# Optimization experiments

Hardware: AMD Instinct MI355X
Metric: run time of the kernel (lower is better)

Reference implementation:

```python
import jax, jax.numpy as jnp
import numpy as np

N = 20000
E = 320000
IN_C, HID, OUT_C = 128, 64, 32
H12, H3 = 4, 1  # heads for conv1/conv2 and conv3
NEG_SLOPE = 0.2


def _glorot(key, shape):
    fan_in, fan_out = shape[0], shape[-1]
    lim = (6.0 / (fan_in + fan_out)) ** 0.5
    return jax.random.uniform(key, shape, jnp.float32, -lim, lim)


def setup_inputs() -> dict:
    key = jax.random.key(0)
    ks = jax.random.split(key, 16)
    x = jax.random.normal(ks[0], (N, IN_C), jnp.float32)
    edge_index = jax.random.randint(ks[1], (2, E), 0, N, jnp.int64)
    p = {
        'W1': _glorot(ks[2], (IN_C, H12 * HID)),
        'as1': _glorot(ks[3], (H12, HID)), 'ad1': _glorot(ks[4], (H12, HID)),
        'b1': jnp.zeros((HID,), jnp.float32),
        'W2': _glorot(ks[5], (HID, H12 * HID)),
        'as2': _glorot(ks[6], (H12, HID)), 'ad2': _glorot(ks[7], (H12, HID)),
        'b2': jnp.zeros((HID,), jnp.float32),
        'W3': _glorot(ks[8], (HID, H3 * OUT_C)),
        'as3': _glorot(ks[9], (H3, OUT_C)), 'ad3': _glorot(ks[10], (H3, OUT_C)),
        'b3': jnp.zeros((OUT_C,), jnp.float32),
        'Wm': _glorot(ks[11], (OUT_C, OUT_C)), 'bm': jnp.zeros((OUT_C,), jnp.float32),
        'Wv': _glorot(ks[12], (OUT_C, OUT_C)), 'bv': jnp.zeros((OUT_C,), jnp.float32),
    }
    return dict(x=x, edge_index=edge_index, **p)


def gat_layer(x, src, dst, W, a_src, a_dst, b, heads, out_c):
    # x: [N, in_c] -> h: [N, H, C]
    h = (x @ W).reshape(-1, heads, out_c)
    alpha_s = jnp.einsum('nhc,hc->nh', h, a_src)  # [N,H]
    alpha_d = jnp.einsum('nhc,hc->nh', h, a_dst)
    e = jax.nn.leaky_relu(alpha_s[src] + alpha_d[dst], NEG_SLOPE)  # [E',H]
    # segment softmax over incoming edges of each dst node
    m = jax.ops.segment_max(e, dst, num_segments=N)
    p = jnp.exp(e - m[dst])
    s = jax.ops.segment_sum(p, dst, num_segments=N)
    alpha = p / (s[dst] + 1e-16)  # [E',H]
    msg = h[src] * alpha[:, :, None]  # [E',H,C]
    out = jax.ops.segment_sum(msg, dst, num_segments=N)  # [N,H,C]
    return out.mean(axis=1) + b  # concat=False -> mean over heads


def reference(x, edge_index, W1, as1, ad1, b1, W2, as2, ad2, b2,
              W3, as3, ad3, b3, Wm, bm, Wv, bv):
    # PyG GATConv default: add self loops
    loop = jnp.arange(N, dtype=edge_index.dtype)
    src = jnp.concatenate([edge_index[0], loop])
    dst = jnp.concatenate([edge_index[1], loop])

    h = jax.nn.relu(gat_layer(x, src, dst, W1, as1, ad1, b1, H12, HID))
    h = jax.nn.relu(gat_layer(h, src, dst, W2, as2, ad2, b2, H12, HID))
    z = gat_layer(h, src, dst, W3, as3, ad3, b3, H3, OUT_C)

    z_mean = z @ Wm + bm
    z_var = jnp.clip(jnp.exp(z @ Wv + bv), 1e-8, 100.0)
    return (z_mean, z_var, z)
```

## Files before the change

### kernel.cpp

```cpp
#include <hip/hip_runtime.h>
#include <hip/hip_bf16.h>

typedef unsigned short ushortT;
typedef short short8 __attribute__((ext_vector_type(8)));
typedef unsigned short ushort8v __attribute__((ext_vector_type(8)));
typedef float float4v __attribute__((ext_vector_type(4)));

constexpr int Nn   = 20000;
constexpr int Ee   = 320000;
constexpr int EP   = Ee + Nn;
constexpr float NSL = 0.2f;
constexpr int CAP  = 128;

__device__ __forceinline__ float b2f(__hip_bfloat16 v) { return __bfloat162float(v); }
__device__ __forceinline__ float bits2f(unsigned short u) {
    __hip_bfloat16 b; *(unsigned short*)&b = u; return __bfloat162float(b);
}
__device__ __forceinline__ unsigned short f2bits(float v) {
    __hip_bfloat16 b = __float2bfloat16(v); return *(unsigned short*)&b;
}
__device__ __forceinline__ float ldf(const void* p, size_t i, int bf) {
    return bf ? __bfloat162float(((const __hip_bfloat16*)p)[i])
              : ((const float*)p)[i];
}
__device__ __forceinline__ void stf(void* p, size_t i, float v, int bf) {
    if (bf) ((__hip_bfloat16*)p)[i] = __float2bfloat16(v);
    else    ((float*)p)[i] = v;
}

__global__ void probe_k(const int* __restrict__ ei, const unsigned* __restrict__ xbits,
                        int* __restrict__ eflag, int* __restrict__ fflag,
                        int* __restrict__ cnt) {
    int gi = blockIdx.x * 256 + threadIdx.x;
    if (gi < Nn) cnt[gi] = 0;
    if (blockIdx.x != 0) return;
    __shared__ int bad, c_s;
    if (threadIdx.x == 0) { bad = 0; c_s = 0; }
    __syncthreads();
    for (int i = threadIdx.x; i < 1024; i += 256)
        if (ei[2 * i + 1] != 0) bad = 1;
    int c = 0;
    for (int i = threadIdx.x; i < 512; i += 256) {
        unsigned e = (xbits[i] >> 7) & 0xFFu;
        if (e >= 110u && e <= 135u) ++c;
    }
    atomicAdd(&c_s, c);
    __syncthreads();
    if (threadIdx.x == 0) {
        *eflag = bad ? 0 : 1;
        *fflag = (c_s > 384) ? 1 : 0;
    }
}

__device__ __forceinline__ void load_edge(const int* __restrict__ ei, int sh, int e,
                                          int& si, int& di) {
    if (e < Ee) {
        si = ei[(size_t)e << sh];
        di = ei[(size_t)(Ee + e) << sh];
    } else {
        si = di = e - Ee;
    }
}

__global__ void prep_k(const void* __restrict__ W1, const void* __restrict__ W2,
                       ushortT* __restrict__ WT1, ushortT* __restrict__ WT2,
                       const int* __restrict__ fflag) {
    const int bf = *fflag;
    int idx = blockIdx.x * 256 + threadIdx.x;
    if (idx < 256 * 128) {
        int j = idx >> 7, k = idx & 127;
        WT1[idx] = f2bits(ldf(W1, (size_t)k * 256 + j, bf));
    } else {
        int i2 = idx - 256 * 128;
        if (i2 < 256 * 64) {
            int j = i2 >> 6, k = i2 & 63;
            WT2[i2] = f2bits(ldf(W2, (size_t)k * 256 + j, bf));
        }
    }
}

__global__ void scatter_k(const int* __restrict__ ei, const int* __restrict__ eflag,
                          int* __restrict__ cnt, int* __restrict__ csr) {
    int e = blockIdx.x * 256 + threadIdx.x;
    if (e >= EP) return;
    int sh = *eflag, si, di;
    load_edge(ei, sh, e, si, di);
    int pos = atomicAdd(cnt + di, 1);
    if (pos < CAP) csr[di * CAP + pos] = si;
}

template <int XMODE, int INC>
__global__ __launch_bounds__(256) void gemm_mfma(const void* __restrict__ xg,
                                                 const ushortT* __restrict__ WT,
                                                 ushortT* __restrict__ h,
                                                 const void* __restrict__ avs,
                                                 const void* __restrict__ avd,
                                                 float* __restrict__ as_, float* __restrict__ ad_,
                                                 const int* __restrict__ fflag) {
    constexpr int SW = INC + 8, SX = INC + 8, CPR = INC / 8;
    const int bf  = *fflag;
    const int xbf = (XMODE == 0) ? bf : 1;
    __shared__ ushortT wt_s[128 * SW];
    __shared__ ushortT xs[64 * SX];
    __shared__ float av_s[2][128];
    const int base = blockIdx.x * 64;
    const int jh   = blockIdx.y;
    const ushortT* WTg = WT + (size_t)jh * 128 * INC;
    for (int ch = threadIdx.x; ch < 128 * CPR; ch += 256) {
        int j = ch / CPR, kc = (ch - j * CPR) * 8;
        *(short8*)(wt_s + j * SW + kc) = *(const short8*)(WTg + j * INC + kc);
    }
    for (int ch = threadIdx.x; ch < 64 * CPR; ch += 256) {
        int nl = ch / CPR, kc = (ch - nl * CPR) * 8;
        int node = base + nl;
        short8 v = {0, 0, 0, 0, 0, 0, 0, 0};
        if (node < Nn) {
            if (xbf) {
                v = *(const short8*)((const ushortT*)xg + (size_t)node * INC + kc);
            } else {
                const float* xf = (const float*)xg + (size_t)node * INC + kc;
#pragma unroll
                for (int i = 0; i < 8; ++i) v[i] = (short)f2bits(xf[i]);
            }
        }
        *(short8*)(xs + nl * SX + kc) = v;
    }
    if (threadIdx.x < 128) {
        av_s[0][threadIdx.x] = ldf(avs, jh * 128 + threadIdx.x, bf);
        av_s[1][threadIdx.x] = ldf(avd, jh * 128 + threadIdx.x, bf);
    }
    __syncthreads();
    const int lane = threadIdx.x & 63, w = threadIdx.x >> 6;
    const int ln = lane & 15, quad = lane >> 4;
    float4v acc[8];
#pragma unroll
    for (int T = 0; T < 8; ++T) acc[T] = (float4v){0.f, 0.f, 0.f, 0.f};
#pragma unroll
    for (int ks = 0; ks < INC / 32; ++ks) {
        const int kb = ks * 32 + quad * 8;
        const short8 b = *(const short8*)(xs + (w * 16 + ln) * SX + kb);
#pragma unroll
        for (int T = 0; T < 8; ++T) {
            const short8 a = *(const short8*)(wt_s + (T * 16 + ln) * SW + kb);
            acc[T] = __builtin_amdgcn_mfma_f32_16x16x32_bf16(a, b, acc[T], 0, 0, 0);
        }
    }
    const int node = base + w * 16 + ln;
    const bool live = (node < Nn);
    ushortT* hn = h + (size_t)node * 256 + jh * 128;
    float pas0 = 0, pas1 = 0, pad0 = 0, pad1 = 0;
#pragma unroll
    for (int T = 0; T < 8; ++T) {
        const int jl = T * 16 + quad * 4;
        ushort4 pk;
        pk.x = f2bits(acc[T][0]); pk.y = f2bits(acc[T][1]);
        pk.z = f2bits(acc[T][2]); pk.w = f2bits(acc[T][3]);
        if (live) *(ushort4*)(hn + jl) = pk;
#pragma unroll
        for (int r = 0; r < 4; ++r) {
            const float v = acc[T][r];
            const float was = av_s[0][jl + r], wad = av_s[1][jl + r];
            if (T < 4) { pas0 = fmaf(v, was, pas0); pad0 = fmaf(v, wad, pad0); }
            else       { pas1 = fmaf(v, was, pas1); pad1 = fmaf(v, wad, pad1); }
        }
    }
#pragma unroll
    for (int off = 16; off < 64; off <<= 1) {
        pas0 += __shfl_xor(pas0, off, 64);
        pas1 += __shfl_xor(pas1, off, 64);
        pad0 += __shfl_xor(pad0, off, 64);
        pad1 += __shfl_xor(pad1, off, 64);
    }
    if (lane < 16 && live) {
        as_[node * 4 + jh * 2]     = pas0;
        as_[node * 4 + jh * 2 + 1] = pas1;
        ad_[node * 4 + jh * 2]     = pad0;
        ad_[node * 4 + jh * 2 + 1] = pad1;
    }
}

__global__ __launch_bounds__(256) void gemm_small(const float* __restrict__ x,
                                                  const void* __restrict__ W,
                                                  __hip_bfloat16* __restrict__ h,
                                                  const void* __restrict__ avs,
                                                  const void* __restrict__ avd,
                                                  float* __restrict__ as_, float* __restrict__ ad_,
                                                  const int* __restrict__ fflag, int N) {
    constexpr int INC = 64, R = 32, PAD = R + 4;
    const int bf = *fflag;
    __shared__ float xsh[INC * PAD];
    int base = blockIdx.x * R;
    for (int i = threadIdx.x; i < R * INC; i += 256) {
        int rr = i / INC, kk = i - rr * INC;
        int nn = base + rr;
        xsh[kk * PAD + rr] = (nn < N) ? x[(size_t)nn * INC + kk] : 0.0f;
    }
    __syncthreads();
    const int jc = threadIdx.x & 31;
    const int g  = threadIdx.x >> 5;
    float acc[4] = {};
    if (bf) {
        const __hip_bfloat16* Wb = (const __hip_bfloat16*)W;
#pragma unroll 4
        for (int k = 0; k < INC; ++k) {
            float4 xv = *(const float4*)(xsh + k * PAD + g * 4);
            float w = b2f(Wb[k * 32 + jc]);
            acc[0] = fmaf(xv.x, w, acc[0]);
            acc[1] = fmaf(xv.y, w, acc[1]);
            acc[2] = fmaf(xv.z, w, acc[2]);
            acc[3] = fmaf(xv.w, w, acc[3]);
        }
    } else {
        const float* Wf = (const float*)W;
#pragma unroll 4
        for (int k = 0; k < INC; ++k) {
            float4 xv = *(const float4*)(xsh + k * PAD + g * 4);
            float w = Wf[k * 32 + jc];
            acc[0] = fmaf(xv.x, w, acc[0]);
            acc[1] = fmaf(xv.y, w, acc[1]);
            acc[2] = fmaf(xv.z, w, acc[2]);
            acc[3] = fmaf(xv.w, w, acc[3]);
        }
    }
    float avsr = ldf(avs, jc, bf), avdr = ldf(avd, jc, bf);
#pragma unroll
    for (int m = 0; m < 4; ++m) {
        int n = base + g * 4 + m;
        if (n >= N) continue;
        h[(size_t)n * 32 + jc] = __float2bfloat16(acc[m]);
        float t1 = acc[m] * avsr;
        float t2 = acc[m] * avdr;
#pragma unroll
        for (int off = 16; off > 0; off >>= 1) {
            t1 += __shfl_down(t1, off, 32);
            t2 += __shfl_down(t2, off, 32);
        }
        if (jc == 0) { as_[n] = t1; ad_[n] = t2; }
    }
}

template <bool RELU>
__global__ __launch_bounds__(256) void aggr4_k(const int* __restrict__ cnt,
                                               const int* __restrict__ csr,
                                               const float* __restrict__ as_,
                                               const float* __restrict__ ad_,
                                               const unsigned short* __restrict__ h,
                                               const void* __restrict__ bias,
                                               const int* __restrict__ fflag,
                                               float* __restrict__ outF,
                                               ushortT* __restrict__ outB, int N) {
    const int lane = threadIdx.x & 63, seg = threadIdx.x >> 6;
    int d = blockIdx.x * 4 + seg;
    if (d >= N) return;
    const int deg = min(cnt[d], CAP);
    const int base = d * CAP;
    const float4 adv = *(const float4*)(ad_ + d * 4);
    const int hl = lane >> 5, cl = lane & 31;
    const int q = cl >> 3, c8 = (cl & 7) * 8;
    float a[8] = {0, 0, 0, 0, 0, 0, 0, 0};
    float s0 = 0, s1 = 0, s2 = 0, s3 = 0;

    auto do_edge = [&](int idx) {
        int src = csr[base + idx];
        float4 av = *(const float4*)(as_ + src * 4);
        float v0 = av.x + adv.x; v0 = v0 > 0.f ? v0 : NSL * v0; float e0 = __expf(v0);
        float v1 = av.y + adv.y; v1 = v1 > 0.f ? v1 : NSL * v1; float e1 = __expf(v1);
        float v2 = av.z + adv.z; v2 = v2 > 0.f ? v2 : NSL * v2; float e2 = __expf(v2);
        float v3 = av.w + adv.w; v3 = v3 > 0.f ? v3 : NSL * v3; float e3 = __expf(v3);
        s0 += e0; s1 += e1; s2 += e2; s3 += e3;
        float ev = (q == 0) ? e0 : (q == 1) ? e1 : (q == 2) ? e2 : e3;
        ushort8v hv = *(const ushort8v*)(h + (size_t)src * 256 + q * 64 + c8);
#pragma unroll
        for (int i = 0; i < 8; ++i) a[i] = fmaf(ev, bits2f(hv[i]), a[i]);
    };

    int e = 0;
    for (; e + 8 <= deg; e += 8) {
        do_edge(e + hl);
        do_edge(e + 2 + hl);
        do_edge(e + 4 + hl);
        do_edge(e + 6 + hl);
    }
    for (; e + 2 <= deg; e += 2) do_edge(e + hl);
    if (e < deg && hl == 0) do_edge(e);

    s0 += __shfl_xor(s0, 32, 64);
    s1 += __shfl_xor(s1, 32, 64);
    s2 += __shfl_xor(s2, 32, 64);
    s3 += __shfl_xor(s3, 32, 64);
    const float sq = (q == 0) ? s0 : (q == 1) ? s1 : (q == 2) ? s2 : s3;
    const float iq = 0.25f / (sq + 1e-16f);
#pragma unroll
    for (int i = 0; i < 8; ++i) {
        a[i] *= iq;
        a[i] += __shfl_xor(a[i], 32, 64);
        a[i] += __shfl_xor(a[i], 8, 64);
        a[i] += __shfl_xor(a[i], 16, 64);
    }
    if (lane < 8) {
        const int bf = *fflag;
        float r[8];
#pragma unroll
        for (int i = 0; i < 8; ++i) {
            r[i] = a[i] + ldf(bias, lane * 8 + i, bf);
            if (RELU) r[i] = fmaxf(r[i], 0.f);
        }
        if (outF) {
            *(float4*)(outF + (size_t)d * 64 + lane * 8)     = make_float4(r[0], r[1], r[2], r[3]);
            *(float4*)(outF + (size_t)d * 64 + lane * 8 + 4) = make_float4(r[4], r[5], r[6], r[7]);
        }
        if (outB) {
            ushort8v p;
#pragma unroll
            for (int i = 0; i < 8; ++i) p[i] = f2bits(r[i]);
            *(ushort8v*)(outB + (size_t)d * 64 + lane * 8) = p;
        }
    }
}

__global__ __launch_bounds__(256) void aggr1f_k(const int* __restrict__ cnt,
                                                const int* __restrict__ csr,
                                                const float* __restrict__ as_,
                                                const float* __restrict__ ad_,
                                                const __hip_bfloat16* __restrict__ h,
                                                const void* __restrict__ b3,
                                                const void* __restrict__ Wm,
                                                const void* __restrict__ bm,
                                                const void* __restrict__ Wv,
                                                const void* __restrict__ bv,
                                                const int* __restrict__ fflag,
                                                void* __restrict__ out, int N) {
    __shared__ float wm_s[1024], wv_s[1024];
    const int bf = *fflag;
    for (int i = threadIdx.x; i < 1024; i += 256) {
        wm_s[i] = ldf(Wm, i, bf);
        wv_s[i] = ldf(Wv, i, bf);
    }
    __syncthreads();
    const int c = threadIdx.x & 31, seg = threadIdx.x >> 5;
    const int d = blockIdx.x * 8 + seg;
    if (d >= N) return;
    const int deg = min(cnt[d], CAP);
    const int base = d * CAP;
    const float advd = ad_[d];
    float s = 0, acc = 0;

    auto do_edge1 = [&](int idx) {
        int src = csr[base + idx];
        float v = as_[src] + advd;
        v = v > 0.f ? v : NSL * v;
        float ev = __expf(v);
        s += ev;
        acc = fmaf(ev, b2f(h[src * 32 + c]), acc);
    };
    int e = 0;
    for (; e + 4 <= deg; e += 4) {
        do_edge1(e); do_edge1(e + 1); do_edge1(e + 2); do_edge1(e + 3);
    }
    for (; e < deg; ++e) do_edge1(e);

    const float inv = 1.0f / (s + 1e-16f);
    const float z = inv * acc + ldf(b3, c, bf);
    stf(out, (size_t)2 * N * 32 + (size_t)d * 32 + c, z, bf);
    float sm = ldf(bm, c, bf), sv = ldf(bv, c, bf);
#pragma unroll 8
    for (int k = 0; k < 32; ++k) {
        float zk = __shfl(z, k, 32);
        sm = fmaf(zk, wm_s[k * 32 + c], sm);
        sv = fmaf(zk, wv_s[k * 32 + c], sv);
    }
    float var = __expf(sv);
    var = fminf(fmaxf(var, 1e-8f), 100.0f);
    stf(out, (size_t)d * 32 + c, sm, bf);
    stf(out, (size_t)N * 32 + (size_t)d * 32 + c, var, bf);
}

extern "C" void kernel_launch(void* const* d_in, const int* in_sizes, int n_in,
                              void* d_out, int out_size, void* d_ws, size_t ws_size,
                              hipStream_t stream) {
    const void* x   = d_in[0];
    const int*  ei  = (const int*)d_in[1];
    const void* W1  = d_in[2];
    const void* as1 = d_in[3];
    const void* ad1 = d_in[4];
    const void* b1  = d_in[5];
    const void* W2  = d_in[6];
    const void* as2 = d_in[7];
    const void* ad2 = d_in[8];
    const void* b2  = d_in[9];
    const void* W3  = d_in[10];
    const void* as3 = d_in[11];
    const void* ad3 = d_in[12];
    const void* b3  = d_in[13];
    const void* Wm  = d_in[14];
    const void* bm  = d_in[15];
    const void* Wv  = d_in[16];
    const void* bv  = d_in[17];

    float* ws = (float*)d_ws;
    ushortT* h    = (ushortT*)ws;
    ushortT* x1b  = (ushortT*)(ws + 2560000);
    float*  x2    = ws + 3200000;
    float*  as_   = ws + 4480000;
    float*  ad_   = ws + 4560000;
    ushortT* WT1  = (ushortT*)(ws + 4640000);
    ushortT* WT2  = (ushortT*)(ws + 4656384);
    int*    cnt   = (int*)(ws + 4664576);
    int*    csr   = (int*)(ws + 4684576);
    int*    eflag = (int*)(ws + 7244576);
    int*    fflag = (int*)(ws + 7244577);

    probe_k<<<79, 256, 0, stream>>>(ei, (const unsigned*)x, eflag, fflag, cnt);
    prep_k<<<192, 256, 0, stream>>>(W1, W2, WT1, WT2, fflag);
    scatter_k<<<(EP + 255) / 256, 256, 0, stream>>>(ei, eflag, cnt, csr);

    dim3 gg(313, 2);
    gemm_mfma<0, 128><<<gg, 256, 0, stream>>>(x, WT1, h, as1, ad1, as_, ad_, fflag);
    aggr4_k<true><<<5000, 256, 0, stream>>>(cnt, csr, as_, ad_, h, b1, fflag,
                                            nullptr, x1b, Nn);

    gemm_mfma<1, 64><<<gg, 256, 0, stream>>>(x1b, WT2, h, as2, ad2, as_, ad_, fflag);
    aggr4_k<true><<<5000, 256, 0, stream>>>(cnt, csr, as_, ad_, h, b2, fflag,
                                            x2, nullptr, Nn);

    gemm_small<<<625, 256, 0, stream>>>(x2, W3, (__hip_bfloat16*)h, as3, ad3, as_, ad_, fflag, Nn);
    aggr1f_k<<<2500, 256, 0, stream>>>(cnt, csr, as_, ad_, (const __hip_bfloat16*)h,
                                       b3, Wm, bm, Wv, bv, fflag, d_out, Nn);
}
```

Before: 254.8 us.

## Precompute per-edge attention weights in LDS before gather-accumulate in aggregation kernels

Both aggregation kernels now use a first pass, with one lane per edge, that loads the source indices and computes the exponentiated attention scores. The scores (and, in the last layer, the row offsets) go into shared memory, and the exponent sums are reduced across the wavefront. This removes the redundant per-lane recomputation of exp and the repeated csr/alpha loads in the feature gather loop, so each lane only fetches the features and does FMAs. It costs extra LDS, and in aggr4_k there are cross-lane shuffles to pick up source indices. Neither kernel syncs between the LDS write and read, which relies on each wave accessing only its own LDS slice.

```diff
diff --git a/kernel.cpp b/kernel.cpp
--- a/kernel.cpp
+++ b/kernel.cpp
@@ -249,45 +249,66 @@
                                                const int* __restrict__ fflag,
                                                float* __restrict__ outF,
                                                ushortT* __restrict__ outB, int N) {
+    __shared__ float lal[4][CAP][4];
     const int lane = threadIdx.x & 63, seg = threadIdx.x >> 6;
     int d = blockIdx.x * 4 + seg;
     if (d >= N) return;
     const int deg = min(cnt[d], CAP);
     const int base = d * CAP;
     const float4 adv = *(const float4*)(ad_ + d * 4);
-    const int hl = lane >> 5, cl = lane & 31;
-    const int q = cl >> 3, c8 = (cl & 7) * 8;
-    float a[8] = {0, 0, 0, 0, 0, 0, 0, 0};
+    const int src0 = (lane < deg) ? csr[base + lane] : 0;
+    const int src1 = (64 + lane < deg) ? csr[base + 64 + lane] : 0;
     float s0 = 0, s1 = 0, s2 = 0, s3 = 0;
-
-    auto do_edge = [&](int idx) {
-        int src = csr[base + idx];
-        float4 av = *(const float4*)(as_ + src * 4);
+    if (lane < deg) {
+        float4 av = *(const float4*)(as_ + src0 * 4);
         float v0 = av.x + adv.x; v0 = v0 > 0.f ? v0 : NSL * v0; float e0 = __expf(v0);
         float v1 = av.y + adv.y; v1 = v1 > 0.f ? v1 : NSL * v1; float e1 = __expf(v1);
         float v2 = av.z + adv.z; v2 = v2 > 0.f ? v2 : NSL * v2; float e2 = __expf(v2);
         float v3 = av.w + adv.w; v3 = v3 > 0.f ? v3 : NSL * v3; float e3 = __expf(v3);
         s0 += e0; s1 += e1; s2 += e2; s3 += e3;
-        float ev = (q == 0) ? e0 : (q == 1) ? e1 : (q == 2) ? e2 : e3;
-        ushort8v hv = *(const ushort8v*)(h + (size_t)src * 256 + q * 64 + c8);
+        *(float4*)(&lal[seg][lane][0]) = make_float4(e0, e1, e2, e3);
+    }
+    if (64 + lane < deg) {
+        float4 av = *(const float4*)(as_ + src1 * 4);
+        float v0 = av.x + adv.x; v0 = v0 > 0.f ? v0 : NSL * v0; float e0 = __expf(v0);
+        float v1 = av.y + adv.y; v1 = v1 > 0.f ? v1 : NSL * v1; float e1 = __expf(v1);
+        float v2 = av.z + adv.z; v2 = v2 > 0.f ? v2 : NSL * v2; float e2 = __expf(v2);
+        float v3 = av.w + adv.w; v3 = v3 > 0.f ? v3 : NSL * v3; float e3 = __expf(v3);
+        s0 += e0; s1 += e1; s2 += e2; s3 += e3;
+        *(float4*)(&lal[seg][64 + lane][0]) = make_float4(e0, e1, e2, e3);
+    }
+    const int hl = lane >> 5, cl = lane & 31;
+    const int q = cl >> 3, c8 = (cl & 7) * 8;
+    const float* lal_s = &lal[seg][0][0];
+    float a[8] = {0, 0, 0, 0, 0, 0, 0, 0};
+
+    auto do_edge = [&](int idx, bool valid) {
+        int sa = __shfl(src0, idx & 63, 64);
+        int sb = __shfl(src1, idx & 63, 64);
+        int src = (idx < 64) ? sa : sb;
+        float ev = valid ? lal_s[idx * 4 + q] : 0.0f;
+        int off = valid ? src * 256 : 0;
+        ushort8v hv = *(const ushort8v*)(h + off + q * 64 + c8);
 #pragma unroll
         for (int i = 0; i < 8; ++i) a[i] = fmaf(ev, bits2f(hv[i]), a[i]);
     };
 
     int e = 0;
     for (; e + 8 <= deg; e += 8) {
-        do_edge(e + hl);
-        do_edge(e + 2 + hl);
-        do_edge(e + 4 + hl);
-        do_edge(e + 6 + hl);
-    }
-    for (; e + 2 <= deg; e += 2) do_edge(e + hl);
-    if (e < deg && hl == 0) do_edge(e);
-
-    s0 += __shfl_xor(s0, 32, 64);
-    s1 += __shfl_xor(s1, 32, 64);
-    s2 += __shfl_xor(s2, 32, 64);
-    s3 += __shfl_xor(s3, 32, 64);
+        do_edge(e + hl, true);
+        do_edge(e + 2 + hl, true);
+        do_edge(e + 4 + hl, true);
+        do_edge(e + 6 + hl, true);
+    }
+    for (; e < deg; e += 2) do_edge(e + hl, (e + hl) < deg);
+
+#pragma unroll
+    for (int off = 1; off < 64; off <<= 1) {
+        s0 += __shfl_xor(s0, off, 64);
+        s1 += __shfl_xor(s1, off, 64);
+        s2 += __shfl_xor(s2, off, 64);
+        s3 += __shfl_xor(s3, off, 64);
+    }
     const float sq = (q == 0) ? s0 : (q == 1) ? s1 : (q == 2) ? s2 : s3;
     const float iq = 0.25f / (sq + 1e-16f);
 #pragma unroll
@@ -331,6 +352,8 @@
                                                 const int* __restrict__ fflag,
                                                 void* __restrict__ out, int N) {
     __shared__ float wm_s[1024], wv_s[1024];
+    __shared__ float lal[8][CAP];
+    __shared__ int   lof[8][CAP];
     const int bf = *fflag;
     for (int i = threadIdx.x; i < 1024; i += 256) {
         wm_s[i] = ldf(Wm, i, bf);
@@ -343,22 +366,33 @@
     const int deg = min(cnt[d], CAP);
     const int base = d * CAP;
     const float advd = ad_[d];
-    float s = 0, acc = 0;
-
-    auto do_edge1 = [&](int idx) {
-        int src = csr[base + idx];
+    float s = 0;
+    for (int i = c; i < deg; i += 32) {
+        int src = csr[base + i];
         float v = as_[src] + advd;
         v = v > 0.f ? v : NSL * v;
         float ev = __expf(v);
         s += ev;
-        acc = fmaf(ev, b2f(h[src * 32 + c]), acc);
-    };
+        lal[seg][i] = ev;
+        lof[seg][i] = src * 32;
+    }
+    float acc = 0.0f;
     int e = 0;
     for (; e + 4 <= deg; e += 4) {
-        do_edge1(e); do_edge1(e + 1); do_edge1(e + 2); do_edge1(e + 3);
-    }
-    for (; e < deg; ++e) do_edge1(e);
-
+        float ev0 = lal[seg][e], ev1 = lal[seg][e + 1];
+        float ev2 = lal[seg][e + 2], ev3 = lal[seg][e + 3];
+        int o0 = lof[seg][e], o1 = lof[seg][e + 1];
+        int o2 = lof[seg][e + 2], o3 = lof[seg][e + 3];
+        float h0 = b2f(h[o0 + c]), h1 = b2f(h[o1 + c]);
+        float h2 = b2f(h[o2 + c]), h3 = b2f(h[o3 + c]);
+        acc = fmaf(ev0, h0, acc);
+        acc = fmaf(ev1, h1, acc);
+        acc = fmaf(ev2, h2, acc);
+        acc = fmaf(ev3, h3, acc);
+    }
+    for (; e < deg; ++e) acc = fmaf(lal[seg][e], b2f(h[lof[seg][e] + c]), acc);
+#pragma unroll
+    for (int off = 1; off < 32; off <<= 1) s += __shfl_xor(s, off, 32);
     const float inv = 1.0f / (s + 1e-16f);
     const float z = inv * acc + ldf(b3, c, bf);
     stf(out, (size_t)2 * N * 32 + (size_t)d * 32 + c, z, bf);
```

Measured after the change: 221.1 us. -13.2%, faster.
